# Kernel tuning notes

Hardware: AMD Instinct MI355X
Metric: run time of the kernel (lower is better)

Reference implementation:

```python
import jax, jax.numpy as jnp
import numpy as np

B, S, D, H, L, E, FF = 16, 1024, 384, 8, 3, 8, 768
DH = D // H
TOP_K = 2


def _ln(x, s, b):
    m = x.mean(-1, keepdims=True)
    v = x.var(-1, keepdims=True)
    return (x - m) * jax.lax.rsqrt(v + 1e-5) * s + b


def setup_inputs() -> dict:
    key = jax.random.key(0)
    ks = jax.random.split(key, 12)
    def n(k, shp, scale=0.02):
        return jax.random.normal(k, shp, jnp.float32) * scale
    return dict(
        x=jax.random.normal(ks[0], (B, S, 1), jnp.float32),
        proj_w=n(ks[1], (1, D)), proj_b=jnp.zeros((D,), jnp.float32),
        qkv_w=n(ks[2], (L, D, 3 * D)), qkv_b=jnp.zeros((L, 3 * D), jnp.float32),
        out_w=n(ks[3], (L, D, D)), out_b=jnp.zeros((L, D), jnp.float32),
        n1_s=jnp.ones((L, D), jnp.float32), n1_b=jnp.zeros((L, D), jnp.float32),
        n2_s=jnp.ones((L, D), jnp.float32), n2_b=jnp.zeros((L, D), jnp.float32),
        gate_w=n(ks[4], (L, D, E)),
        e_w1=n(ks[5], (L, E, D, FF)), e_b1=jnp.zeros((L, E, FF), jnp.float32),
        e_w2=n(ks[6], (L, E, FF, D)), e_b2=jnp.zeros((L, E, D), jnp.float32),
        att_w=n(ks[7], (D,)), att_b=jnp.zeros((), jnp.float32),
        head_w=n(ks[8], (D, 1)), head_b=jnp.zeros((1,), jnp.float32),
    )


def reference(x, proj_w, proj_b, qkv_w, qkv_b, out_w, out_b,
              n1_s, n1_b, n2_s, n2_b, gate_w, e_w1, e_b1, e_w2, e_b2,
              att_w, att_b, head_w, head_b):
    # feature projection: [B,S,1] -> [B,S,D]
    h = x @ proj_w + proj_b
    total_moe = jnp.zeros((), h.dtype)
    scale = np.float32(1.0 / np.sqrt(DH))
    for l in range(L):
        # --- pre-norm multi-head self-attention ---
        xn = _ln(h, n1_s[l], n1_b[l])
        qkv = xn @ qkv_w[l] + qkv_b[l]
        q, k, v = jnp.split(qkv, 3, axis=-1)
        q = q.reshape(B, S, H, DH)
        k = k.reshape(B, S, H, DH)
        v = v.reshape(B, S, H, DH)
        attn = jax.nn.softmax(jnp.einsum('bqhd,bkhd->bhqk', q, k) * scale, axis=-1)
        ao = jnp.einsum('bhqk,bkhd->bqhd', attn, v).reshape(B, S, D)
        h = h + (ao @ out_w[l] + out_b[l])
        # --- pre-norm top-2 gated MoE FFN ---
        xn2 = _ln(h, n2_s[l], n2_b[l])
        probs = jax.nn.softmax(xn2 @ gate_w[l], axis=-1)            # [B,S,E]
        topv, topi = jax.lax.top_k(probs, TOP_K)
        gates = topv / topv.sum(-1, keepdims=True)                  # renormalized top-2
        full = (jax.nn.one_hot(topi, E, dtype=h.dtype) * gates[..., None]).sum(-2)  # [B,S,E]
        moe_out = jnp.zeros_like(h)
        for e in range(E):  # fixed small expert loop
            ye = jax.nn.relu(xn2 @ e_w1[l, e] + e_b1[l, e]) @ e_w2[l, e] + e_b2[l, e]
            moe_out = moe_out + full[..., e:e + 1] * ye
        h = h + moe_out
        # switch-style load-balancing aux loss
        importance = probs.reshape(-1, E).mean(0)
        load = (full > 0).astype(h.dtype).reshape(-1, E).mean(0)
        total_moe = total_moe + E * jnp.sum(importance * load)
    w = jax.nn.softmax(h @ att_w + att_b, axis=1)                   # [B,S]
    pooled = jnp.einsum('bs,bsd->bd', w, h)
    rul = pooled @ head_w + head_b                                  # [B,1]
    return rul, total_moe
```

## Files before the change

### kernel.cpp

```cpp
#include <hip/hip_runtime.h>
#include <hip/hip_bf16.h>
#include <math.h>

#define TOKENS 16384
#define DMODEL 384
#define SEQ 1024
#define NHEAD 8
#define DHEAD 48
#define NEXP 8
#define FFDIM 768
#define NL 3

typedef __bf16 bf16x8 __attribute__((ext_vector_type(8)));
typedef __bf16 bf16x4 __attribute__((ext_vector_type(4)));
typedef float f32x4 __attribute__((ext_vector_type(4)));

__global__ void init_kernel(float* total_moe) { *total_moe = 0.f; }

__global__ void zero_cnt_kernel(int* counts, float* sum_probs) {
  int t = threadIdx.x;
  if (t < NEXP) { counts[t] = 0; sum_probs[t] = 0.f; }
}

__global__ void finalize_kernel(const float* total_moe, float* out) { out[16] = *total_moe; }

__global__ __launch_bounds__(256) void proj_kernel(const float* __restrict__ x,
    const float* __restrict__ pw, const float* __restrict__ pb, float* __restrict__ h) {
  int i = blockIdx.x * 256 + threadIdx.x;
  int t = i / DMODEL;
  int d = i - t * DMODEL;
  h[i] = x[t] * pw[d] + pb[d];
}

__global__ __launch_bounds__(256) void convw_kernel(const float* __restrict__ src,
    __bf16* __restrict__ dst, int K, int N) {
  __shared__ float t[32][33];
  size_t boff = (size_t)blockIdx.z * K * N;
  src += boff; dst += boff;
  int k0 = blockIdx.y * 32, n0 = blockIdx.x * 32;
  int tx = threadIdx.x & 31, ty = threadIdx.x >> 5;
#pragma unroll
  for (int i = 0; i < 32; i += 8) t[ty + i][tx] = src[(size_t)(k0 + ty + i) * N + n0 + tx];
  __syncthreads();
#pragma unroll
  for (int i = 0; i < 32; i += 8)
    dst[(size_t)(n0 + ty + i) * K + k0 + tx] = (__bf16)t[tx][ty + i];
}

__global__ __launch_bounds__(384) void ln_kernel(const float* __restrict__ src,
    __bf16* __restrict__ dst, const float* __restrict__ gs, const float* __restrict__ gb) {
  int row = blockIdx.x, tid = threadIdx.x;
  float v = src[(size_t)row * DMODEL + tid];
  float sum = v, sq = v * v;
#pragma unroll
  for (int off = 32; off; off >>= 1) { sum += __shfl_xor(sum, off); sq += __shfl_xor(sq, off); }
  __shared__ float rs[6], rq[6];
  __shared__ float smean, sinv;
  int wid = tid >> 6;
  if ((tid & 63) == 0) { rs[wid] = sum; rq[wid] = sq; }
  __syncthreads();
  if (tid == 0) {
    float S = 0.f, Q = 0.f;
    for (int w = 0; w < 6; w++) { S += rs[w]; Q += rq[w]; }
    float mean = S / (float)DMODEL;
    float var = Q / (float)DMODEL - mean * mean;
    smean = mean; sinv = rsqrtf(var + 1e-5f);
  }
  __syncthreads();
  dst[(size_t)row * DMODEL + tid] = (__bf16)((v - smean) * sinv * gs[tid] + gb[tid]);
}

template<int MODE>
__global__ __launch_bounds__(256) void mgemm_kernel(
    const __bf16* __restrict__ Abf, const __bf16* __restrict__ Wt,
    const float* __restrict__ bias, float* __restrict__ Cf, __bf16* __restrict__ Cb,
    __bf16* __restrict__ pQ, __bf16* __restrict__ pK, __bf16* __restrict__ pV,
    const int* __restrict__ counts, const int* __restrict__ offs,
    const int* __restrict__ tok_list, const float* __restrict__ gate_list,
    int N, int K) {
  int e = 0, cnt = 0, base = 0;
  const int* tl = nullptr;
  int m0 = blockIdx.y * 128;
  int n0 = blockIdx.x * 128;
  if constexpr (MODE == 2 || MODE == 3) {
    e = blockIdx.z;
    cnt = counts[e];
    if (m0 >= cnt) return;
    base = offs[e];
    tl = tok_list + e * TOKENS;
    Wt += (size_t)e * N * K;
    bias += (size_t)e * N;
  }
  __shared__ __align__(16) __bf16 As[2][128][72];
  __shared__ __align__(16) __bf16 Bs[2][128][72];
  int tid = threadIdx.x;
  int w = tid >> 6, lane = tid & 63, c = lane & 15, g = lane >> 4;
  int arow[4], acol[4];
#pragma unroll
  for (int i = 0; i < 4; i++) {
    int chunk = tid + 256 * i;
    arow[i] = chunk >> 3;
    acol[i] = (chunk & 7) * 8;
  }
  long tok[4];
#pragma unroll
  for (int i = 0; i < 4; i++) {
    int mr = m0 + arow[i];
    if constexpr (MODE == 2)      tok[i] = (mr < cnt) ? (long)(tl[mr] & 0xFFFF) : -1;
    else if constexpr (MODE == 3) tok[i] = (mr < cnt) ? (long)(base + mr) : -1;
    else                          tok[i] = mr;
  }
  f32x4 acc[2][8];
#pragma unroll
  for (int m = 0; m < 2; m++)
#pragma unroll
    for (int n = 0; n < 8; n++) { acc[m][n][0] = 0.f; acc[m][n][1] = 0.f; acc[m][n][2] = 0.f; acc[m][n][3] = 0.f; }

  bf16x8 ra[4], rb[4];
  int nk = K >> 6;
#pragma unroll
  for (int i = 0; i < 4; i++) {
    bf16x8 v = {};
    if (tok[i] >= 0) v = *(const bf16x8*)&Abf[(size_t)tok[i] * K + acol[i]];
    ra[i] = v;
    rb[i] = *(const bf16x8*)&Wt[(size_t)(n0 + arow[i]) * K + acol[i]];
  }
  for (int kt = 0; kt < nk; kt++) {
    int cb = kt & 1;
#pragma unroll
    for (int i = 0; i < 4; i++) {
      *(bf16x8*)&As[cb][arow[i]][acol[i]] = ra[i];
      *(bf16x8*)&Bs[cb][arow[i]][acol[i]] = rb[i];
    }
    __syncthreads();
    if (kt + 1 < nk) {
      int k0 = (kt + 1) << 6;
#pragma unroll
      for (int i = 0; i < 4; i++) {
        bf16x8 v = {};
        if (tok[i] >= 0) v = *(const bf16x8*)&Abf[(size_t)tok[i] * K + k0 + acol[i]];
        ra[i] = v;
        rb[i] = *(const bf16x8*)&Wt[(size_t)(n0 + arow[i]) * K + k0 + acol[i]];
      }
    }
#pragma unroll
    for (int kk = 0; kk < 2; kk++) {
      bf16x8 a0 = *(const bf16x8*)&As[cb][w * 32 + c][kk * 32 + g * 8];
      bf16x8 a1 = *(const bf16x8*)&As[cb][w * 32 + 16 + c][kk * 32 + g * 8];
#pragma unroll
      for (int n = 0; n < 8; n++) {
        bf16x8 b = *(const bf16x8*)&Bs[cb][n * 16 + c][kk * 32 + g * 8];
        acc[0][n] = __builtin_amdgcn_mfma_f32_16x16x32_bf16(a0, b, acc[0][n], 0, 0, 0);
        acc[1][n] = __builtin_amdgcn_mfma_f32_16x16x32_bf16(a1, b, acc[1][n], 0, 0, 0);
      }
    }
  }
  if constexpr (MODE == 0 || MODE == 1) {
#pragma unroll
    for (int m = 0; m < 2; m++) {
      int row = w * 32 + m * 16 + 4 * g;
#pragma unroll
      for (int n = 0; n < 8; n++) {
        int col = n0 + n * 16 + c;
        float bv = bias[col];
#pragma unroll
        for (int r = 0; r < 4; r++) {
          float v = acc[m][n][r] + bv;
          int lr = row + r;
          if constexpr (MODE == 0) {
            int t = m0 + lr;
            int b = t >> 10, s = t & 1023;
            int which = col / 384;
            int rem = col - which * 384;
            int hd = rem / 48;
            int d = rem - hd * 48;
            size_t bh = (size_t)(b * 8 + hd);
            if (which == 0)      pQ[(bh * 1024 + s) * 48 + d] = (__bf16)(v * 0.20823510262f);
            else if (which == 1) pK[(bh * 1024 + s) * 48 + d] = (__bf16)v;
            else                 pV[(bh * 48 + d) * 1024 + s] = (__bf16)v;
          } else {
            Cf[(size_t)(m0 + lr) * N + col] += v;
          }
        }
      }
    }
  } else {
    __syncthreads();
    __bf16* Ct = &As[0][0][0];
    const int CSTR = 130;
    float rowg[2][4];
    if constexpr (MODE == 3) {
#pragma unroll
      for (int m = 0; m < 2; m++)
#pragma unroll
        for (int r = 0; r < 4; r++) {
          int row = m0 + w * 32 + m * 16 + 4 * g + r;
          rowg[m][r] = (row < cnt) ? gate_list[e * TOKENS + row] : 0.f;
        }
    }
#pragma unroll
    for (int m = 0; m < 2; m++) {
      int row = w * 32 + m * 16 + 4 * g;
#pragma unroll
      for (int n = 0; n < 8; n++) {
        int col = n * 16 + c;
        float bv = bias[n0 + col];
#pragma unroll
        for (int r = 0; r < 4; r++) {
          float v = acc[m][n][r] + bv;
          if constexpr (MODE == 2) v = fmaxf(v, 0.f);
          else v *= rowg[m][r];
          Ct[(row + r) * CSTR + col] = (__bf16)v;
        }
      }
    }
    __syncthreads();
    int row = tid >> 1, half = tid & 1;
    int mr = m0 + row;
    if (mr < cnt) {
      const __bf16* srcl = &Ct[row * CSTR + half * 64];
      __bf16* dst;
      if constexpr (MODE == 2) {
        dst = &Cb[(size_t)(base + mr) * N + n0 + half * 64];
      } else {
        int entry = tl[mr];
        int t = entry & 0xFFFF, a = entry >> 16;
        dst = &Cb[((size_t)a * TOKENS + t) * DMODEL + n0 + half * 64];
      }
#pragma unroll
      for (int i = 0; i < 8; i++) *(bf16x8*)&dst[i * 8] = *(const bf16x8*)&srcl[i * 8];
    }
  }
}

__global__ __launch_bounds__(256) void combine_kernel(float* __restrict__ h,
    const __bf16* __restrict__ ab) {
  size_t i = ((size_t)blockIdx.x * 256 + threadIdx.x) * 8;
  bf16x8 a0 = *(const bf16x8*)&ab[i];
  bf16x8 a1 = *(const bf16x8*)&ab[(size_t)TOKENS * DMODEL + i];
  float* hp = h + i;
#pragma unroll
  for (int j = 0; j < 8; j++) hp[j] += (float)a0[j] + (float)a1[j];
}

__global__ __launch_bounds__(256) void attn_kernel(const __bf16* __restrict__ Qh,
    const __bf16* __restrict__ Kh, const __bf16* __restrict__ VTh,
    __bf16* __restrict__ ao) {
  __shared__ __align__(16) __bf16 Ks[64][72];
  __shared__ __align__(16) __bf16 Vt[48][72];
  __shared__ __align__(16) __bf16 Ps[4][16][72];
  int bh = blockIdx.x;
  int q0 = blockIdx.y * 64;
  int tid = threadIdx.x;
  int w = tid >> 6, lane = tid & 63, c = lane & 15, g = lane >> 4;

  for (int i = tid; i < 192; i += 256) {
    int row = i / 3, seg = i - row * 3;
    bf16x8 z = {};
    *(bf16x8*)&Ks[row][48 + seg * 8] = z;
  }

  const __bf16* qrow = Qh + ((size_t)bh * 1024 + q0 + w * 16 + c) * 48;
  bf16x8 qb0 = *(const bf16x8*)&qrow[g * 8];
  bf16x8 qb1 = {};
  if (g < 2) qb1 = *(const bf16x8*)&qrow[32 + g * 8];

  const __bf16* kb = Kh + (size_t)bh * 1024 * 48;
  const __bf16* vb = VTh + (size_t)bh * 48 * 1024;

  int r0 = tid / 6, p0 = tid - r0 * 6;
  __bf16* dst0 = &Ks[r0][p0 * 8];
  int off0 = r0 * 48 + p0 * 8;
  int e1 = tid + 256;
  __bf16* dst1; int off1; bool v1;
  if (e1 < 384) { int r = e1 / 6, p = e1 - r * 6; dst1 = &Ks[r][p * 8]; off1 = r * 48 + p * 8; v1 = false; }
  else          { int i = e1 - 384; int d = i >> 3, p = i & 7; dst1 = &Vt[d][p * 8]; off1 = d * 1024 + p * 8; v1 = true; }
  int i2 = tid + 512 - 384;
  int d2 = i2 >> 3, p2 = i2 & 7;
  __bf16* dst2 = &Vt[d2][p2 * 8];
  int off2 = d2 * 1024 + p2 * 8;

  f32x4 acc[3];
#pragma unroll
  for (int t = 0; t < 3; t++) { acc[t][0] = 0.f; acc[t][1] = 0.f; acc[t][2] = 0.f; acc[t][3] = 0.f; }
  f32x4 lacc = {};
  bf16x8 ones;
#pragma unroll
  for (int j = 0; j < 8; j++) ones[j] = (__bf16)1.0f;

  for (int kt = 0; kt < 16; kt++) {
    __syncthreads();
    const __bf16* kbt = kb + (size_t)kt * 3072;
    const __bf16* vbt = vb + kt * 64;
    *(bf16x8*)dst0 = *(const bf16x8*)(kbt + off0);
    *(bf16x8*)dst1 = *(const bf16x8*)((v1 ? vbt : kbt) + off1);
    *(bf16x8*)dst2 = *(const bf16x8*)(vbt + off2);
    __syncthreads();

    f32x4 s4[4];
#pragma unroll
    for (int f = 0; f < 4; f++) {
      bf16x8 ka0 = *(const bf16x8*)&Ks[f * 16 + c][g * 8];
      bf16x8 ka1 = *(const bf16x8*)&Ks[f * 16 + c][32 + g * 8];
      f32x4 z = {};
      z = __builtin_amdgcn_mfma_f32_16x16x32_bf16(ka0, qb0, z, 0, 0, 0);
      s4[f] = __builtin_amdgcn_mfma_f32_16x16x32_bf16(ka1, qb1, z, 0, 0, 0);
    }
#pragma unroll
    for (int f = 0; f < 4; f++) {
      float pv0 = __builtin_amdgcn_exp2f(s4[f][0]);
      float pv1 = __builtin_amdgcn_exp2f(s4[f][1]);
      float pv2 = __builtin_amdgcn_exp2f(s4[f][2]);
      float pv3 = __builtin_amdgcn_exp2f(s4[f][3]);
      bf16x4 pk = { (__bf16)pv0, (__bf16)pv1, (__bf16)pv2, (__bf16)pv3 };
      *(bf16x4*)&Ps[w][c][f * 16 + 4 * g] = pk;
    }
    bf16x8 pa0 = *(const bf16x8*)&Ps[w][c][g * 8];
    bf16x8 pa1 = *(const bf16x8*)&Ps[w][c][32 + g * 8];
#pragma unroll
    for (int t = 0; t < 3; t++) {
      bf16x8 vb0 = *(const bf16x8*)&Vt[t * 16 + c][g * 8];
      bf16x8 vb1 = *(const bf16x8*)&Vt[t * 16 + c][32 + g * 8];
      acc[t] = __builtin_amdgcn_mfma_f32_16x16x32_bf16(pa0, vb0, acc[t], 0, 0, 0);
      acc[t] = __builtin_amdgcn_mfma_f32_16x16x32_bf16(pa1, vb1, acc[t], 0, 0, 0);
    }
    lacc = __builtin_amdgcn_mfma_f32_16x16x32_bf16(pa0, ones, lacc, 0, 0, 0);
    lacc = __builtin_amdgcn_mfma_f32_16x16x32_bf16(pa1, ones, lacc, 0, 0, 0);
  }
  float linv[4];
#pragma unroll
  for (int r = 0; r < 4; r++) linv[r] = 1.f / lacc[r];
  int b = bh >> 3, hh = bh & 7;
#pragma unroll
  for (int t = 0; t < 3; t++)
#pragma unroll
    for (int r = 0; r < 4; r++)
      ao[((size_t)(b * SEQ + q0 + w * 16 + 4 * g + r)) * DMODEL + hh * 48 + t * 16 + c] =
          (__bf16)(acc[t][r] * linv[r]);
}

__global__ __launch_bounds__(256) void gate_kernel(const __bf16* __restrict__ xnb,
    const float* __restrict__ gw, int* __restrict__ counts, float* __restrict__ sum_probs,
    int* __restrict__ tok_list, float* __restrict__ gate_list) {
  __shared__ float Gs[NEXP][DMODEL];
  __shared__ float simp[NEXP];
  __shared__ int hist[NEXP], basep[NEXP];
  __shared__ unsigned char tokE[32][2];
  __shared__ float tokG[32][2];
  __shared__ short rankS[32][2];
  int tid = threadIdx.x;
  for (int i = tid; i < DMODEL * NEXP; i += 256) {
    int d = i >> 3, e2 = i & 7;
    Gs[e2][d] = gw[i];
  }
  if (tid < NEXP) { simp[tid] = 0.f; hist[tid] = 0; }
  __syncthreads();
  int w = tid >> 6, lane = tid & 63;
  int tbase = blockIdx.x * 32 + w * 8;
  float impacc[NEXP] = {};
  for (int tt = 0; tt < 8; tt++) {
    int t = tbase + tt;
    float p[NEXP] = {};
#pragma unroll
    for (int j = 0; j < 6; j++) {
      int d = lane + 64 * j;
      float xv = (float)xnb[(size_t)t * DMODEL + d];
#pragma unroll
      for (int e2 = 0; e2 < NEXP; e2++) p[e2] += xv * Gs[e2][d];
    }
#pragma unroll
    for (int off = 32; off; off >>= 1)
#pragma unroll
      for (int e2 = 0; e2 < NEXP; e2++) p[e2] += __shfl_xor(p[e2], off);
    float mx = p[0];
#pragma unroll
    for (int e2 = 1; e2 < NEXP; e2++) mx = fmaxf(mx, p[e2]);
    float s = 0.f;
#pragma unroll
    for (int e2 = 0; e2 < NEXP; e2++) { p[e2] = __expf(p[e2] - mx); s += p[e2]; }
    float inv = 1.f / s;
#pragma unroll
    for (int e2 = 0; e2 < NEXP; e2++) { p[e2] *= inv; impacc[e2] += p[e2]; }
    int i0 = 0; float v0 = p[0];
#pragma unroll
    for (int e2 = 1; e2 < NEXP; e2++) if (p[e2] > v0) { v0 = p[e2]; i0 = e2; }
    int i1 = -1; float v1 = -INFINITY;
#pragma unroll
    for (int e2 = 0; e2 < NEXP; e2++) if (e2 != i0 && p[e2] > v1) { v1 = p[e2]; i1 = e2; }
    if (lane == 0) {
      float gsum = v0 + v1;
      int r0 = atomicAdd(&hist[i0], 1);
      int r1 = atomicAdd(&hist[i1], 1);
      int sl = w * 8 + tt;
      tokE[sl][0] = (unsigned char)i0; tokE[sl][1] = (unsigned char)i1;
      tokG[sl][0] = v0 / gsum;         tokG[sl][1] = v1 / gsum;
      rankS[sl][0] = (short)r0;        rankS[sl][1] = (short)r1;
    }
  }
  if (lane == 0)
#pragma unroll
    for (int e2 = 0; e2 < NEXP; e2++) atomicAdd(&simp[e2], impacc[e2]);
  __syncthreads();
  if (tid < NEXP) {
    basep[tid] = atomicAdd(&counts[tid], hist[tid]);
    atomicAdd(&sum_probs[tid], simp[tid]);
  }
  __syncthreads();
  int t0 = blockIdx.x * 32;
  if (tid < 64) {
    int sl = tid >> 1, a = tid & 1;
    int e2 = tokE[sl][a];
    int pos = basep[e2] + rankS[sl][a];
    tok_list[e2 * TOKENS + pos] = (t0 + sl) | (a << 16);
    gate_list[e2 * TOKENS + pos] = tokG[sl][a];
  }
}

__global__ void aux_kernel(const int* __restrict__ counts, int* __restrict__ offs,
                           const float* __restrict__ sum_probs, float* __restrict__ total_moe) {
  int off = 0;
  float tm = 0.f;
  for (int e = 0; e < NEXP; e++) {
    offs[e] = off;
    off += ((counts[e] + 63) >> 6) << 6;
    tm += sum_probs[e] * (float)counts[e];
  }
  offs[NEXP] = off;
  *total_moe += (float)NEXP * tm / ((float)TOKENS * (float)TOKENS);
}

__global__ __launch_bounds__(256) void head1_kernel(const float* __restrict__ h,
    const float* __restrict__ att_w, const float* __restrict__ att_b,
    float* __restrict__ logits) {
  int tid = threadIdx.x;
  int w = tid >> 6, lane = tid & 63;
  float4 aw0 = *(const float4*)&att_w[lane * 4];
  float2 aw1 = *(const float2*)&att_w[256 + lane * 2];
  float ab = att_b[0];
  for (int i = w; i < 32; i += 4) {
    int t = blockIdx.x * 32 + i;
    const float* hr = h + (size_t)t * DMODEL;
    float4 v4 = *(const float4*)&hr[lane * 4];
    float2 v2 = *(const float2*)&hr[256 + lane * 2];
    float dot = v4.x * aw0.x + v4.y * aw0.y + v4.z * aw0.z + v4.w * aw0.w
              + v2.x * aw1.x + v2.y * aw1.y;
#pragma unroll
    for (int off = 32; off; off >>= 1) dot += __shfl_xor(dot, off);
    if (lane == 0) logits[t] = dot + ab;
  }
}

__global__ __launch_bounds__(256) void head2_kernel(float* __restrict__ logits) {
  int b = blockIdx.x, tid = threadIdx.x;
  int w = tid >> 6, lane = tid & 63;
  float* lb = logits + b * SEQ;
  __shared__ float red[4];
  float lv[4];
  float mx = -INFINITY;
#pragma unroll
  for (int i = 0; i < 4; i++) { lv[i] = lb[tid + 256 * i]; mx = fmaxf(mx, lv[i]); }
#pragma unroll
  for (int off = 32; off; off >>= 1) mx = fmaxf(mx, __shfl_xor(mx, off));
  if (lane == 0) red[w] = mx;
  __syncthreads();
  mx = fmaxf(fmaxf(red[0], red[1]), fmaxf(red[2], red[3]));
  __syncthreads();
  float s = 0.f;
#pragma unroll
  for (int i = 0; i < 4; i++) { lv[i] = __expf(lv[i] - mx); s += lv[i]; }
#pragma unroll
  for (int off = 32; off; off >>= 1) s += __shfl_xor(s, off);
  if (lane == 0) red[w] = s;
  __syncthreads();
  float inv = 1.f / (red[0] + red[1] + red[2] + red[3]);
#pragma unroll
  for (int i = 0; i < 4; i++) lb[tid + 256 * i] = lv[i] * inv;
}

__global__ __launch_bounds__(256) void head3a_kernel(const float* __restrict__ h,
    const float* __restrict__ wnorm, float* __restrict__ partial) {
  int b = blockIdx.x, dc = blockIdx.y, sc = blockIdx.z;
  int tid = threadIdx.x;
  int d = tid & 63, sg = tid >> 6;
  const float* hb = h + (size_t)b * SEQ * DMODEL + dc * 64 + d;
  const float* wb = wnorm + b * SEQ + sc * 64;
  float acc = 0.f;
  int s0 = sc * 64 + sg * 16;
#pragma unroll
  for (int i = 0; i < 16; i++)
    acc += wb[sg * 16 + i] * hb[(size_t)(s0 + i) * DMODEL];
  __shared__ float red[256];
  red[tid] = acc;
  __syncthreads();
  if (sg == 0)
    partial[(((size_t)b * 6 + dc) * 16 + sc) * 64 + d] =
        red[d] + red[64 + d] + red[128 + d] + red[192 + d];
}

__global__ void head3b_kernel(const float* __restrict__ partial,
    const float* __restrict__ head_w, float* __restrict__ part) {
  int b = blockIdx.x, dc = blockIdx.y;
  int d = threadIdx.x;
  const float* pp = partial + (((size_t)b * 6 + dc) * 16) * 64 + d;
  float pooled = 0.f;
#pragma unroll
  for (int sc = 0; sc < 16; sc++) pooled += pp[sc * 64];
  float pd = pooled * head_w[dc * 64 + d];
#pragma unroll
  for (int off = 32; off; off >>= 1) pd += __shfl_xor(pd, off);
  if (d == 0) part[b * 6 + dc] = pd;
}

__global__ void head4_kernel(const float* __restrict__ part,
                             const float* __restrict__ head_b, float* __restrict__ out) {
  int b = threadIdx.x;
  if (b < 16) {
    float s = head_b[0];
#pragma unroll
    for (int dc = 0; dc < 6; dc++) s += part[b * 6 + dc];
    out[b] = s;
  }
}

extern "C" void kernel_launch(void* const* d_in, const int* in_sizes, int n_in,
                              void* d_out, int out_size, void* d_ws, size_t ws_size,
                              hipStream_t stream) {
  (void)in_sizes; (void)n_in; (void)out_size; (void)ws_size;
  const float* x      = (const float*)d_in[0];
  const float* proj_w = (const float*)d_in[1];
  const float* proj_b = (const float*)d_in[2];
  const float* qkv_w  = (const float*)d_in[3];
  const float* qkv_b  = (const float*)d_in[4];
  const float* out_w  = (const float*)d_in[5];
  const float* out_b  = (const float*)d_in[6];
  const float* n1_s   = (const float*)d_in[7];
  const float* n1_b   = (const float*)d_in[8];
  const float* n2_s   = (const float*)d_in[9];
  const float* n2_b   = (const float*)d_in[10];
  const float* gate_w = (const float*)d_in[11];
  const float* e_w1   = (const float*)d_in[12];
  const float* e_b1   = (const float*)d_in[13];
  const float* e_w2   = (const float*)d_in[14];
  const float* e_b2   = (const float*)d_in[15];
  const float* att_w  = (const float*)d_in[16];
  const float* att_b  = (const float*)d_in[17];
  const float* head_w = (const float*)d_in[18];
  const float* head_b = (const float*)d_in[19];
  float* out = (float*)d_out;

  char* wsb = (char*)d_ws;
  float*  h    = (float*)(wsb);
  __bf16* xnb  = (__bf16*)(wsb + 25165824);
  __bf16* aob  = (__bf16*)(wsb + 37748736);
  __bf16* ab   = (__bf16*)(wsb + 25165824);
  __bf16* uni  = (__bf16*)(wsb + 50331648);
  __bf16* Qh   = uni;
  __bf16* Khd  = (__bf16*)(wsb + 62914560);
  __bf16* VTh  = (__bf16*)(wsb + 75497472);
  __bf16* qkvWt = (__bf16*)(wsb + 101449728);
  __bf16* outWt = (__bf16*)(wsb + 104103936);
  __bf16* e1Wt  = (__bf16*)(wsb + 104988672);
  __bf16* e2Wt  = (__bf16*)(wsb + 119144448);
  char* sm = wsb + 133300224;
  int*   counts    = (int*)(sm);
  int*   offs      = (int*)(sm + 64);
  float* sum_probs = (float*)(sm + 128);
  float* total_moe = (float*)(sm + 192);
  int*   tok_list  = (int*)(sm + 256);
  float* gate_list = (float*)(sm + 256 + 524288);
  float* logits    = (float*)(sm + 1048832);
  float* part      = (float*)(sm + 1048832 + 65536);
  float* partial   = (float*)(sm + 1048832 + 131072);

  convw_kernel<<<dim3(36, 12, 3), 256, 0, stream>>>(qkv_w, qkvWt, 384, 1152);
  convw_kernel<<<dim3(12, 12, 3), 256, 0, stream>>>(out_w, outWt, 384, 384);
  convw_kernel<<<dim3(24, 12, 24), 256, 0, stream>>>(e_w1, e1Wt, 384, 768);
  convw_kernel<<<dim3(12, 24, 24), 256, 0, stream>>>(e_w2, e2Wt, 768, 384);

  init_kernel<<<1, 1, 0, stream>>>(total_moe);
  proj_kernel<<<TOKENS * DMODEL / 256, 256, 0, stream>>>(x, proj_w, proj_b, h);

  for (int l = 0; l < NL; l++) {
    ln_kernel<<<TOKENS, 384, 0, stream>>>(h, xnb, n1_s + l * DMODEL, n1_b + l * DMODEL);
    mgemm_kernel<0><<<dim3(9, 128), 256, 0, stream>>>(
        xnb, qkvWt + (size_t)l * 1152 * 384, qkv_b + l * 1152, nullptr, nullptr,
        Qh, Khd, VTh, nullptr, nullptr, nullptr, nullptr, 1152, 384);
    attn_kernel<<<dim3(128, 16), 256, 0, stream>>>(Qh, Khd, VTh, aob);
    mgemm_kernel<1><<<dim3(3, 128), 256, 0, stream>>>(
        aob, outWt + (size_t)l * 384 * 384, out_b + l * 384, h, nullptr,
        nullptr, nullptr, nullptr, nullptr, nullptr, nullptr, nullptr, 384, 384);
    ln_kernel<<<TOKENS, 384, 0, stream>>>(h, xnb, n2_s + l * DMODEL, n2_b + l * DMODEL);
    zero_cnt_kernel<<<1, 64, 0, stream>>>(counts, sum_probs);
    gate_kernel<<<512, 256, 0, stream>>>(xnb, gate_w + (size_t)l * DMODEL * NEXP,
                                         counts, sum_probs, tok_list, gate_list);
    aux_kernel<<<1, 1, 0, stream>>>(counts, offs, sum_probs, total_moe);
    mgemm_kernel<2><<<dim3(6, 128, 8), 256, 0, stream>>>(
        xnb, e1Wt + (size_t)l * 8 * 768 * 384, e_b1 + l * 8 * FFDIM, nullptr, uni,
        nullptr, nullptr, nullptr, counts, offs, tok_list, nullptr, 768, 384);
    mgemm_kernel<3><<<dim3(3, 128, 8), 256, 0, stream>>>(
        uni, e2Wt + (size_t)l * 8 * 384 * 768, e_b2 + l * 8 * DMODEL, nullptr, ab,
        nullptr, nullptr, nullptr, counts, offs, tok_list, gate_list, 384, 768);
    combine_kernel<<<TOKENS * DMODEL / (256 * 8), 256, 0, stream>>>(h, ab);
  }

  head1_kernel<<<512, 256, 0, stream>>>(h, att_w, att_b, logits);
  head2_kernel<<<16, 256, 0, stream>>>(logits);
  head3a_kernel<<<dim3(16, 6, 16), 256, 0, stream>>>(h, logits, partial);
  head3b_kernel<<<dim3(16, 6), 64, 0, stream>>>(partial, head_w, part);
  head4_kernel<<<1, 64, 0, stream>>>(part, head_b, out);
  finalize_kernel<<<1, 1, 0, stream>>>(total_moe, out);
}
```

Baseline: 995.4 us.

## Process two 64-query tiles per attention block to reuse K/V tiles

Each attention block now handles 128 queries (two 16-row groups per wave) instead of 64, so each K/V tile loaded into shared memory serves twice as many queries, and the grid shrinks by half. This halves global K/V loads and barrier count per query, at the cost of more registers (two sets of accumulators and Q fragments) and fewer blocks. A launch-bounds hint of 4 blocks per SM caps register use.

```diff
diff --git a/kernel.cpp b/kernel.cpp
--- a/kernel.cpp
+++ b/kernel.cpp
@@ -243,14 +243,14 @@
   for (int j = 0; j < 8; j++) hp[j] += (float)a0[j] + (float)a1[j];
 }
 
-__global__ __launch_bounds__(256) void attn_kernel(const __bf16* __restrict__ Qh,
+__global__ __launch_bounds__(256, 4) void attn_kernel(const __bf16* __restrict__ Qh,
     const __bf16* __restrict__ Kh, const __bf16* __restrict__ VTh,
     __bf16* __restrict__ ao) {
   __shared__ __align__(16) __bf16 Ks[64][72];
   __shared__ __align__(16) __bf16 Vt[48][72];
-  __shared__ __align__(16) __bf16 Ps[4][16][72];
+  __shared__ __align__(16) __bf16 Ps[4][2][16][72];
   int bh = blockIdx.x;
-  int q0 = blockIdx.y * 64;
+  int q0 = blockIdx.y * 128;
   int tid = threadIdx.x;
   int w = tid >> 6, lane = tid & 63, c = lane & 15, g = lane >> 4;
 
@@ -260,10 +260,15 @@
     *(bf16x8*)&Ks[row][48 + seg * 8] = z;
   }
 
-  const __bf16* qrow = Qh + ((size_t)bh * 1024 + q0 + w * 16 + c) * 48;
-  bf16x8 qb0 = *(const bf16x8*)&qrow[g * 8];
-  bf16x8 qb1 = {};
-  if (g < 2) qb1 = *(const bf16x8*)&qrow[32 + g * 8];
+  const __bf16* qrowA = Qh + ((size_t)bh * 1024 + q0 + w * 16 + c) * 48;
+  const __bf16* qrowB = qrowA + 64 * 48;
+  bf16x8 qb0a = *(const bf16x8*)&qrowA[g * 8];
+  bf16x8 qb0b = *(const bf16x8*)&qrowB[g * 8];
+  bf16x8 qb1a = {}, qb1b = {};
+  if (g < 2) {
+    qb1a = *(const bf16x8*)&qrowA[32 + g * 8];
+    qb1b = *(const bf16x8*)&qrowB[32 + g * 8];
+  }
 
   const __bf16* kb = Kh + (size_t)bh * 1024 * 48;
   const __bf16* vb = VTh + (size_t)bh * 48 * 1024;
@@ -280,10 +285,8 @@
   __bf16* dst2 = &Vt[d2][p2 * 8];
   int off2 = d2 * 1024 + p2 * 8;
 
-  f32x4 acc[3];
-#pragma unroll
-  for (int t = 0; t < 3; t++) { acc[t][0] = 0.f; acc[t][1] = 0.f; acc[t][2] = 0.f; acc[t][3] = 0.f; }
-  f32x4 lacc = {};
+  f32x4 accA[3] = {}, accB[3] = {};
+  f32x4 laccA = {}, laccB = {};
   bf16x8 ones;
 #pragma unroll
   for (int j = 0; j < 8; j++) ones[j] = (__bf16)1.0f;
@@ -297,46 +300,52 @@
     *(bf16x8*)dst2 = *(const bf16x8*)(vbt + off2);
     __syncthreads();
 
-    f32x4 s4[4];
 #pragma unroll
     for (int f = 0; f < 4; f++) {
       bf16x8 ka0 = *(const bf16x8*)&Ks[f * 16 + c][g * 8];
       bf16x8 ka1 = *(const bf16x8*)&Ks[f * 16 + c][32 + g * 8];
-      f32x4 z = {};
-      z = __builtin_amdgcn_mfma_f32_16x16x32_bf16(ka0, qb0, z, 0, 0, 0);
-      s4[f] = __builtin_amdgcn_mfma_f32_16x16x32_bf16(ka1, qb1, z, 0, 0, 0);
-    }
-#pragma unroll
-    for (int f = 0; f < 4; f++) {
-      float pv0 = __builtin_amdgcn_exp2f(s4[f][0]);
-      float pv1 = __builtin_amdgcn_exp2f(s4[f][1]);
-      float pv2 = __builtin_amdgcn_exp2f(s4[f][2]);
-      float pv3 = __builtin_amdgcn_exp2f(s4[f][3]);
-      bf16x4 pk = { (__bf16)pv0, (__bf16)pv1, (__bf16)pv2, (__bf16)pv3 };
-      *(bf16x4*)&Ps[w][c][f * 16 + 4 * g] = pk;
-    }
-    bf16x8 pa0 = *(const bf16x8*)&Ps[w][c][g * 8];
-    bf16x8 pa1 = *(const bf16x8*)&Ps[w][c][32 + g * 8];
+      f32x4 za = {}, zb = {};
+      za = __builtin_amdgcn_mfma_f32_16x16x32_bf16(ka0, qb0a, za, 0, 0, 0);
+      f32x4 sa = __builtin_amdgcn_mfma_f32_16x16x32_bf16(ka1, qb1a, za, 0, 0, 0);
+      zb = __builtin_amdgcn_mfma_f32_16x16x32_bf16(ka0, qb0b, zb, 0, 0, 0);
+      f32x4 sb = __builtin_amdgcn_mfma_f32_16x16x32_bf16(ka1, qb1b, zb, 0, 0, 0);
+      bf16x4 pka = { (__bf16)__builtin_amdgcn_exp2f(sa[0]), (__bf16)__builtin_amdgcn_exp2f(sa[1]),
+                     (__bf16)__builtin_amdgcn_exp2f(sa[2]), (__bf16)__builtin_amdgcn_exp2f(sa[3]) };
+      bf16x4 pkb = { (__bf16)__builtin_amdgcn_exp2f(sb[0]), (__bf16)__builtin_amdgcn_exp2f(sb[1]),
+                     (__bf16)__builtin_amdgcn_exp2f(sb[2]), (__bf16)__builtin_amdgcn_exp2f(sb[3]) };
+      *(bf16x4*)&Ps[w][0][c][f * 16 + 4 * g] = pka;
+      *(bf16x4*)&Ps[w][1][c][f * 16 + 4 * g] = pkb;
+    }
+    bf16x8 pa0a = *(const bf16x8*)&Ps[w][0][c][g * 8];
+    bf16x8 pa1a = *(const bf16x8*)&Ps[w][0][c][32 + g * 8];
+    bf16x8 pa0b = *(const bf16x8*)&Ps[w][1][c][g * 8];
+    bf16x8 pa1b = *(const bf16x8*)&Ps[w][1][c][32 + g * 8];
 #pragma unroll
     for (int t = 0; t < 3; t++) {
       bf16x8 vb0 = *(const bf16x8*)&Vt[t * 16 + c][g * 8];
       bf16x8 vb1 = *(const bf16x8*)&Vt[t * 16 + c][32 + g * 8];
-      acc[t] = __builtin_amdgcn_mfma_f32_16x16x32_bf16(pa0, vb0, acc[t], 0, 0, 0);
-      acc[t] = __builtin_amdgcn_mfma_f32_16x16x32_bf16(pa1, vb1, acc[t], 0, 0, 0);
-    }
-    lacc = __builtin_amdgcn_mfma_f32_16x16x32_bf16(pa0, ones, lacc, 0, 0, 0);
-    lacc = __builtin_amdgcn_mfma_f32_16x16x32_bf16(pa1, ones, lacc, 0, 0, 0);
-  }
-  float linv[4];
-#pragma unroll
-  for (int r = 0; r < 4; r++) linv[r] = 1.f / lacc[r];
+      accA[t] = __builtin_amdgcn_mfma_f32_16x16x32_bf16(pa0a, vb0, accA[t], 0, 0, 0);
+      accA[t] = __builtin_amdgcn_mfma_f32_16x16x32_bf16(pa1a, vb1, accA[t], 0, 0, 0);
+      accB[t] = __builtin_amdgcn_mfma_f32_16x16x32_bf16(pa0b, vb0, accB[t], 0, 0, 0);
+      accB[t] = __builtin_amdgcn_mfma_f32_16x16x32_bf16(pa1b, vb1, accB[t], 0, 0, 0);
+    }
+    laccA = __builtin_amdgcn_mfma_f32_16x16x32_bf16(pa0a, ones, laccA, 0, 0, 0);
+    laccA = __builtin_amdgcn_mfma_f32_16x16x32_bf16(pa1a, ones, laccA, 0, 0, 0);
+    laccB = __builtin_amdgcn_mfma_f32_16x16x32_bf16(pa0b, ones, laccB, 0, 0, 0);
+    laccB = __builtin_amdgcn_mfma_f32_16x16x32_bf16(pa1b, ones, laccB, 0, 0, 0);
+  }
+  float linvA[4], linvB[4];
+#pragma unroll
+  for (int r = 0; r < 4; r++) { linvA[r] = 1.f / laccA[r]; linvB[r] = 1.f / laccB[r]; }
   int b = bh >> 3, hh = bh & 7;
 #pragma unroll
   for (int t = 0; t < 3; t++)
 #pragma unroll
-    for (int r = 0; r < 4; r++)
-      ao[((size_t)(b * SEQ + q0 + w * 16 + 4 * g + r)) * DMODEL + hh * 48 + t * 16 + c] =
-          (__bf16)(acc[t][r] * linv[r]);
+    for (int r = 0; r < 4; r++) {
+      size_t rowA = (size_t)(b * SEQ + q0 + w * 16 + 4 * g + r);
+      ao[rowA * DMODEL + hh * 48 + t * 16 + c] = (__bf16)(accA[t][r] * linvA[r]);
+      ao[(rowA + 64) * DMODEL + hh * 48 + t * 16 + c] = (__bf16)(accB[t][r] * linvB[r]);
+    }
 }
 
 __global__ __launch_bounds__(256) void gate_kernel(const __bf16* __restrict__ xnb,
@@ -585,7 +594,7 @@
     mgemm_kernel<0><<<dim3(9, 128), 256, 0, stream>>>(
         xnb, qkvWt + (size_t)l * 1152 * 384, qkv_b + l * 1152, nullptr, nullptr,
         Qh, Khd, VTh, nullptr, nullptr, nullptr, nullptr, 1152, 384);
-    attn_kernel<<<dim3(128, 16), 256, 0, stream>>>(Qh, Khd, VTh, aob);
+    attn_kernel<<<dim3(128, 8), 256, 0, stream>>>(Qh, Khd, VTh, aob);
     mgemm_kernel<1><<<dim3(3, 128), 256, 0, stream>>>(
         aob, outWt + (size_t)l * 384 * 384, out_b + l * 384, h, nullptr,
         nullptr, nullptr, nullptr, nullptr, nullptr, nullptr, nullptr, 384, 384);
```

Result: faster. 955.0 us (-4.1%).
